# Optimization experiments

Measured on AMD Instinct MI355X. Metric: run time of the kernel, lower is better.

Reference implementation:

```python
import jax, jax.numpy as jnp
import numpy as np

NEG_SLOPE = 0.2  # PyG GATConv default leaky_relu slope


def add_self_loops(src, dst, ea, n_nodes):
    # PyG add_self_loops with fill_value='mean': self-loop attr = mean of
    # incoming edge attrs per destination node (0 if no incoming edges).
    cnt = jax.ops.segment_sum(jnp.ones(dst.shape, ea.dtype), dst, num_segments=n_nodes)
    mean_ea = jax.ops.segment_sum(ea, dst, num_segments=n_nodes) / jnp.maximum(cnt, 1.0)[:, None]
    loop = jnp.arange(n_nodes, dtype=src.dtype)
    return (jnp.concatenate([src, loop]),
            jnp.concatenate([dst, loop]),
            jnp.concatenate([ea, mean_ea], axis=0))


def gat_conv(x, src, dst, ea, W, att_src, att_dst, We, att_edge, bias, heads, ch, concat):
    n = x.shape[0]
    xs = (x @ W).reshape(n, heads, ch)                      # [N,H,C]
    a_src = (xs * att_src).sum(-1)                          # [N,H]
    a_dst = (xs * att_dst).sum(-1)                          # [N,H]
    ea_p = (ea @ We).reshape(-1, heads, ch)                 # [E,H,C]
    a_e = (ea_p * att_edge).sum(-1)                         # [E,H]
    logits = jax.nn.leaky_relu(a_src[src] + a_dst[dst] + a_e, NEG_SLOPE)
    m = jax.ops.segment_max(logits, dst, num_segments=n)    # segment softmax over dst
    e = jnp.exp(logits - m[dst])
    denom = jax.ops.segment_sum(e, dst, num_segments=n)
    alpha = e / (denom[dst] + 1e-16)                        # [E,H]
    out = jax.ops.segment_sum(alpha[:, :, None] * xs[src], dst, num_segments=n)  # [N,H,C]
    out = out.reshape(n, heads * ch) if concat else out.mean(axis=1)
    return out + bias


def setup_inputs() -> dict:
    key = jax.random.key(0)
    ks = jax.random.split(key, 14)
    N, E, F_IN, H, C1, C2 = 50000, 800000, 128, 2, 64, 64
    s = 0.05
    return {
        "x": jax.random.normal(ks[0], (N, F_IN), jnp.float32),
        "edge_index": jax.random.randint(ks[1], (2, E), 0, N, jnp.int32),
        "edge_weight": jax.random.uniform(ks[2], (E,), jnp.float32),
        # layer 1 (heads=2, concat=True)
        "W1": jax.random.normal(ks[3], (F_IN, H * C1), jnp.float32) * s,
        "att_src1": jax.random.normal(ks[4], (1, H, C1), jnp.float32) * s,
        "att_dst1": jax.random.normal(ks[5], (1, H, C1), jnp.float32) * s,
        "We1": jax.random.normal(ks[6], (1, H * C1), jnp.float32) * s,
        "att_edge1": jax.random.normal(ks[7], (1, H, C1), jnp.float32) * s,
        "b1": jnp.zeros((H * C1,), jnp.float32),
        # layer 2 (heads=1, concat=False)
        "W2": jax.random.normal(ks[8], (H * C1, C2), jnp.float32) * s,
        "att_src2": jax.random.normal(ks[9], (1, 1, C2), jnp.float32) * s,
        "att_dst2": jax.random.normal(ks[10], (1, 1, C2), jnp.float32) * s,
        "We2": jax.random.normal(ks[11], (1, C2), jnp.float32) * s,
        "att_edge2": jax.random.normal(ks[12], (1, 1, C2), jnp.float32) * s,
        "b2": jnp.zeros((C2,), jnp.float32),
    }


def reference(x, edge_index, edge_weight, W1, att_src1, att_dst1, We1, att_edge1, b1,
              W2, att_src2, att_dst2, We2, att_edge2, b2):
    n = x.shape[0]
    ea = edge_weight[:, None]  # edge_dim=1
    src, dst, ea = add_self_loops(edge_index[0], edge_index[1], ea, n)
    h = gat_conv(x, src, dst, ea, W1, att_src1, att_dst1, We1, att_edge1, b1,
                 heads=2, ch=64, concat=True)
    h = jax.nn.elu(h)
    out = gat_conv(h, src, dst, ea, W2, att_src2, att_dst2, We2, att_edge2, b2,
                   heads=1, ch=64, concat=False)
    return out
```

## Files before the change

### kernel.cpp

```cpp
#include <hip/hip_runtime.h>
#include <math.h>

#define NEG_SLOPE 0.2f

typedef unsigned int u32;
typedef unsigned short u16;
typedef unsigned long long u64;

typedef __attribute__((ext_vector_type(8))) short short8;
typedef __attribute__((ext_vector_type(4))) float f32x4;

__device__ __forceinline__ float bf2f(u16 h) {
  union { u32 u; float f; } c; c.u = ((u32)h) << 16; return c.f;
}
__device__ __forceinline__ u16 f2bf(float f) {
  union { float f; u32 u; } c; c.f = f;
  return (u16)((c.u + 0x7FFFu + ((c.u >> 16) & 1u)) >> 16);
}

__global__ __launch_bounds__(256) void k_hist(const int* __restrict__ dst, int E, int epb,
                                              u32* __restrict__ hist) {
  __shared__ u32 h[256];
  h[threadIdx.x] = 0;
  __syncthreads();
  int b = blockIdx.x;
  int beg = b * epb, end = beg + epb; if (end > E) end = E;
  for (int i = beg + threadIdx.x; i < end; i += 256)
    atomicAdd(&h[(u32)dst[i] >> 8], 1u);
  __syncthreads();
  hist[threadIdx.x * 256 + b] = h[threadIdx.x];
}

__global__ __launch_bounds__(256) void k_scanrow(u32* __restrict__ hist, u32* __restrict__ btot) {
  int bkt = blockIdx.x, t = threadIdx.x;
  u32 orig = hist[bkt * 256 + t];
  u32 v = orig;
  #pragma unroll
  for (int off = 1; off < 64; off <<= 1) {
    u32 u_ = __shfl_up(v, off);
    if ((t & 63) >= off) v += u_;
  }
  __shared__ u32 ws[4];
  if ((t & 63) == 63) ws[t >> 6] = v;
  __syncthreads();
  u32 add = 0; int w = t >> 6;
  if (w > 0) add += ws[0];
  if (w > 1) add += ws[1];
  if (w > 2) add += ws[2];
  u32 incl = v + add;
  hist[bkt * 256 + t] = incl - orig;
  if (t == 255) btot[bkt] = incl;
}

__global__ __launch_bounds__(256) void k_scanb(const u32* __restrict__ btot, u32* __restrict__ bstart) {
  int t = threadIdx.x;
  u32 orig = btot[t];
  u32 v = orig;
  #pragma unroll
  for (int off = 1; off < 64; off <<= 1) {
    u32 u_ = __shfl_up(v, off);
    if ((t & 63) >= off) v += u_;
  }
  __shared__ u32 ws[4];
  if ((t & 63) == 63) ws[t >> 6] = v;
  __syncthreads();
  u32 add = 0; int w = t >> 6;
  if (w > 0) add += ws[0];
  if (w > 1) add += ws[1];
  if (w > 2) add += ws[2];
  u32 incl = v + add;
  bstart[t] = incl - orig;
  if (t == 255) bstart[256] = incl;
}

__global__ __launch_bounds__(256) void k_binscatter(const int* __restrict__ src,
                                                    const int* __restrict__ dst,
                                                    const float* __restrict__ ew,
                                                    const u32* __restrict__ hist,
                                                    const u32* __restrict__ bstart,
                                                    u64* __restrict__ stage, int E, int epb) {
  __shared__ u32 cur[256];
  int b = blockIdx.x;
  cur[threadIdx.x] = bstart[threadIdx.x] + hist[threadIdx.x * 256 + b];
  __syncthreads();
  int beg = b * epb, end = beg + epb; if (end > E) end = E;
  for (int i = beg + threadIdx.x; i < end; i += 256) {
    int d = dst[i];
    u32 bkt = (u32)d >> 8;
    u32 pos = atomicAdd(&cur[bkt], 1u);
    float w = ew[i];
    u32 wq = (u32)(w * 65536.0f); if (wq > 65535u) wq = 65535u;
    stage[pos] = ((u64)((u32)d & 255u) << 32) | ((u64)wq << 16) | (u64)(u32)src[i];
  }
}

__global__ __launch_bounds__(256) void k_bucket(const u64* __restrict__ stage,
                                                const u32* __restrict__ bstart,
                                                u32* __restrict__ col,
                                                u32* __restrict__ ninfo, int n) {
  int bkt = blockIdx.x;
  int beg = (int)bstart[bkt], end = (int)bstart[bkt + 1];
  __shared__ u32 pk[256];
  pk[threadIdx.x] = 0;
  __syncthreads();
  for (int i = beg + threadIdx.x; i < end; i += 256) {
    u64 sv = stage[i];
    u32 ln = (u32)(sv >> 32) & 255u;
    u32 wq = (u32)((sv >> 16) & 0xFFFFu);
    u32 old = atomicAdd(&pk[ln], (1u << 24) | wq);
    u32 rank = old >> 24;
    if (rank < 64u)
      col[((((u32)bkt << 8) + ln) << 6) + rank] = (u32)sv;
  }
  __syncthreads();
  int v = (bkt << 8) + threadIdx.x;
  if (v < n) {
    u32 p = pk[threadIdx.x];
    u32 deg = p >> 24;
    float mean = ((float)(p & 0xFFFFFFu) * (1.0f / 65536.0f)) / (float)(deg > 1 ? deg : 1);
    u32 mq = (u32)(mean * 65536.0f); if (mq > 65535u) mq = 65535u;
    u32 dc = deg > 64u ? 64u : deg;
    ninfo[v] = (dc << 16) | mq;
  }
}

template<int H>
__global__ void k_bfrag(const float* __restrict__ W, uint4* __restrict__ bfrag) {
  int tid = blockIdx.x * 256 + threadIdx.x;
  int f = tid >> 6, lane = tid & 63;
  const int NF = H * 4 * 4 * 2;
  if (f >= NF) return;
  int p = f & 1, t = (f >> 1) & 3, cg = f >> 3;
  int colc = 16 * cg + (lane & 15);
  int k0 = 32 * t + 8 * (lane >> 4);
  u16 v[8];
  #pragma unroll
  for (int j = 0; j < 8; j++) {
    float w = W[(size_t)(k0 + j) * (H * 64) + colc];
    u32 bits = __float_as_uint(w);
    if (p == 0) v[j] = (u16)(bits >> 16);
    else        v[j] = f2bf(w - __uint_as_float(bits & 0xffff0000u));
  }
  uint4 o = { (u32)v[0] | ((u32)v[1] << 16), (u32)v[2] | ((u32)v[3] << 16),
              (u32)v[4] | ((u32)v[5] << 16), (u32)v[6] | ((u32)v[7] << 16) };
  bfrag[f * 64 + lane] = o;
}

template<int H>
__global__ __launch_bounds__(256) void k_gemm_mfma(const float* __restrict__ A,
                                                   const uint4* __restrict__ bfrag,
                                                   u16* __restrict__ xs_bf,
                                                   const float* __restrict__ att_src,
                                                   const float* __restrict__ att_dst,
                                                   float* __restrict__ a_src_out,
                                                   float* __restrict__ a_dst_out,
                                                   int nrows) {
  const int NCG = H * 4;
  int lane = threadIdx.x & 63;
  int wv = threadIdx.x >> 6;
  int lrow = lane & 15, lk = lane >> 4;
  int r0 = blockIdx.x * 64 + wv * 16;
  int arow = r0 + lrow; if (arow > nrows - 1) arow = nrows - 1;
  const float* ap = A + (size_t)arow * 128;

  f32x4 acc[NCG];
  #pragma unroll
  for (int cg = 0; cg < NCG; cg++) acc[cg] = (f32x4){0.f, 0.f, 0.f, 0.f};

  #pragma unroll
  for (int t = 0; t < 4; t++) {
    float4 av0 = *(const float4*)(ap + 32 * t + 8 * lk);
    float4 av1 = *(const float4*)(ap + 32 * t + 8 * lk + 4);
    float af[8] = {av0.x, av0.y, av0.z, av0.w, av1.x, av1.y, av1.z, av1.w};
    short8 ahi, alo;
    #pragma unroll
    for (int j = 0; j < 8; j++) {
      u32 bits = __float_as_uint(af[j]);
      ahi[j] = (short)(bits >> 16);
      alo[j] = (short)f2bf(af[j] - __uint_as_float(bits & 0xffff0000u));
    }
    #pragma unroll
    for (int cg = 0; cg < NCG; cg++) {
      union { uint4 u; short8 s; } bh, bl;
      bh.u = bfrag[((cg * 4 + t) * 2 + 0) * 64 + lane];
      bl.u = bfrag[((cg * 4 + t) * 2 + 1) * 64 + lane];
      acc[cg] = __builtin_amdgcn_mfma_f32_16x16x32_bf16(ahi, bh.s, acc[cg], 0, 0, 0);
      acc[cg] = __builtin_amdgcn_mfma_f32_16x16x32_bf16(ahi, bl.s, acc[cg], 0, 0, 0);
      acc[cg] = __builtin_amdgcn_mfma_f32_16x16x32_bf16(alo, bh.s, acc[cg], 0, 0, 0);
    }
  }

  float ps[2][4], pd[2][4];
  #pragma unroll
  for (int h = 0; h < 2; h++)
    #pragma unroll
    for (int r = 0; r < 4; r++) { ps[h][r] = 0.f; pd[h][r] = 0.f; }

  #pragma unroll
  for (int cg = 0; cg < NCG; cg++) {
    int colbase = 16 * cg + lrow;
    float asv = att_src[colbase];
    float adv = att_dst[colbase];
    const int h = (H == 2) ? (cg >> 2) : 0;
    #pragma unroll
    for (int r = 0; r < 4; r++) {
      ps[h][r] += acc[cg][r] * asv;
      pd[h][r] += acc[cg][r] * adv;
      int row = r0 + 4 * lk + r;
      if (row < nrows) xs_bf[(size_t)row * (H * 64) + colbase] = f2bf(acc[cg][r]);
    }
  }
  #pragma unroll
  for (int h = 0; h < H; h++)
    #pragma unroll
    for (int r = 0; r < 4; r++)
      #pragma unroll
      for (int off = 8; off; off >>= 1) {
        ps[h][r] += __shfl_xor(ps[h][r], off);
        pd[h][r] += __shfl_xor(pd[h][r], off);
      }
  if (lrow == 0) {
    #pragma unroll
    for (int r = 0; r < 4; r++) {
      int row = r0 + 4 * lk + r;
      if (row < nrows) {
        #pragma unroll
        for (int h = 0; h < H; h++) {
          a_src_out[row * H + h] = ps[h][r];
          a_dst_out[row * H + h] = pd[h][r];
        }
      }
    }
  }
}

__global__ void k_scalars(const float* __restrict__ We1, const float* __restrict__ ae1,
                          const float* __restrict__ We2, const float* __restrict__ ae2,
                          float* __restrict__ out) {
  int t = threadIdx.x;
  if (t == 0) { float s = 0; for (int c = 0; c < 64; c++) s += We1[c] * ae1[c]; out[0] = s; }
  if (t == 1) { float s = 0; for (int c = 0; c < 64; c++) s += We1[64 + c] * ae1[64 + c]; out[1] = s; }
  if (t == 2) { float s = 0; for (int c = 0; c < 64; c++) s += We2[c] * ae2[c]; out[2] = s; }
}

__global__ __launch_bounds__(256) void k_agg1(const u32* __restrict__ ninfo,
                                              const u32* __restrict__ col,
                                              const float2* __restrict__ a_src,
                                              const float2* __restrict__ a_dst,
                                              const float* __restrict__ scal,
                                              const u16* __restrict__ xs_bf,
                                              const float* __restrict__ b1,
                                              float* __restrict__ h_out, int n) {
  int wid = (blockIdx.x * 256 + threadIdx.x) >> 4;
  int gl = threadIdx.x & 15;
  if (wid >= n) return;
  u32 nf = ninfo[wid];
  int deg = (int)(nf >> 16);
  float mean = (float)(nf & 0xFFFFu) * (1.0f / 65536.0f);
  float2 ad = a_dst[wid];
  float2 asv_s = a_src[wid];
  float sc0 = scal[0], sc1 = scal[1];
  bool hi = gl >= 8;
  float l0s = asv_s.x + ad.x + mean * sc0;
  float l1s = asv_s.y + ad.y + mean * sc1;
  l0s = l0s > 0.f ? l0s : NEG_SLOPE * l0s;
  l1s = l1s > 0.f ? l1s : NEG_SLOPE * l1s;
  float m0 = l0s, m1 = l1s, den0 = 1.f, den1 = 1.f;
  float acc[8];
  {
    uint4 q = *(const uint4*)&xs_bf[(size_t)wid * 128 + 8 * gl];
    acc[0] = bf2f((u16)q.x); acc[1] = bf2f((u16)(q.x >> 16));
    acc[2] = bf2f((u16)q.y); acc[3] = bf2f((u16)(q.y >> 16));
    acc[4] = bf2f((u16)q.z); acc[5] = bf2f((u16)(q.z >> 16));
    acc[6] = bf2f((u16)q.w); acc[7] = bf2f((u16)(q.w >> 16));
  }
  const u32* cw = col + ((u32)wid << 6);
  for (int p0 = 0; p0 < deg; p0 += 16) {
    int p = p0 + gl;
    bool act = p < deg;
    u32 sw = cw[act ? p : 0];
    int s = (int)(sw & 0xFFFFu);
    float w = (float)(sw >> 16) * (1.0f / 65536.0f);
    float2 asv = a_src[s];
    float l0 = asv.x + ad.x + w * sc0;
    float l1 = asv.y + ad.y + w * sc1;
    l0 = l0 > 0.f ? l0 : NEG_SLOPE * l0;
    l1 = l1 > 0.f ? l1 : NEG_SLOPE * l1;
    if (!act) { l0 = -1e30f; l1 = -1e30f; }
    float cm0 = l0, cm1 = l1;
    #pragma unroll
    for (int off = 8; off; off >>= 1) {
      cm0 = fmaxf(cm0, __shfl_xor(cm0, off, 16));
      cm1 = fmaxf(cm1, __shfl_xor(cm1, off, 16));
    }
    float nm0 = fmaxf(m0, cm0), nm1 = fmaxf(m1, cm1);
    float e0 = __expf(l0 - nm0), e1 = __expf(l1 - nm1);
    float cs0 = e0, cs1 = e1;
    #pragma unroll
    for (int off = 8; off; off >>= 1) {
      cs0 += __shfl_xor(cs0, off, 16);
      cs1 += __shfl_xor(cs1, off, 16);
    }
    float r0 = __expf(m0 - nm0), r1 = __expf(m1 - nm1);
    den0 = den0 * r0 + cs0;
    den1 = den1 * r1 + cs1;
    float rs = hi ? r1 : r0;
    #pragma unroll
    for (int f = 0; f < 8; f++) acc[f] *= rs;
    m0 = nm0; m1 = nm1;
    int cnt = deg - p0; if (cnt > 16) cnt = 16;
    int j = 0;
    for (; j + 2 <= cnt; j += 2) {
      int sj0 = __shfl(s, j, 16);
      int sj1 = __shfl(s, j + 1, 16);
      uint4 qa = *(const uint4*)&xs_bf[(size_t)sj0 * 128 + 8 * gl];
      uint4 qb = *(const uint4*)&xs_bf[(size_t)sj1 * 128 + 8 * gl];
      float a0 = __shfl(e0, j, 16), a1 = __shfl(e1, j, 16);
      float b0 = __shfl(e0, j + 1, 16), b1 = __shfl(e1, j + 1, 16);
      float ala = hi ? a1 : a0;
      float alb = hi ? b1 : b0;
      acc[0] += ala * bf2f((u16)qa.x); acc[1] += ala * bf2f((u16)(qa.x >> 16));
      acc[2] += ala * bf2f((u16)qa.y); acc[3] += ala * bf2f((u16)(qa.y >> 16));
      acc[4] += ala * bf2f((u16)qa.z); acc[5] += ala * bf2f((u16)(qa.z >> 16));
      acc[6] += ala * bf2f((u16)qa.w); acc[7] += ala * bf2f((u16)(qa.w >> 16));
      acc[0] += alb * bf2f((u16)qb.x); acc[1] += alb * bf2f((u16)(qb.x >> 16));
      acc[2] += alb * bf2f((u16)qb.y); acc[3] += alb * bf2f((u16)(qb.y >> 16));
      acc[4] += alb * bf2f((u16)qb.z); acc[5] += alb * bf2f((u16)(qb.z >> 16));
      acc[6] += alb * bf2f((u16)qb.w); acc[7] += alb * bf2f((u16)(qb.w >> 16));
    }
    if (j < cnt) {
      int sj = __shfl(s, j, 16);
      uint4 q = *(const uint4*)&xs_bf[(size_t)sj * 128 + 8 * gl];
      float a0 = __shfl(e0, j, 16), a1 = __shfl(e1, j, 16);
      float al = hi ? a1 : a0;
      acc[0] += al * bf2f((u16)q.x); acc[1] += al * bf2f((u16)(q.x >> 16));
      acc[2] += al * bf2f((u16)q.y); acc[3] += al * bf2f((u16)(q.y >> 16));
      acc[4] += al * bf2f((u16)q.z); acc[5] += al * bf2f((u16)(q.z >> 16));
      acc[6] += al * bf2f((u16)q.w); acc[7] += al * bf2f((u16)(q.w >> 16));
    }
  }
  float inv = 1.f / ((hi ? den1 : den0) + 1e-16f);
  float4 blo = *(const float4*)&b1[8 * gl];
  float4 bhi = *(const float4*)&b1[8 * gl + 4];
  float o[8];
  o[0] = acc[0] * inv + blo.x; o[1] = acc[1] * inv + blo.y;
  o[2] = acc[2] * inv + blo.z; o[3] = acc[3] * inv + blo.w;
  o[4] = acc[4] * inv + bhi.x; o[5] = acc[5] * inv + bhi.y;
  o[6] = acc[6] * inv + bhi.z; o[7] = acc[7] * inv + bhi.w;
  #pragma unroll
  for (int f = 0; f < 8; f++) o[f] = o[f] > 0.f ? o[f] : expm1f(o[f]);
  float* dst = &h_out[(size_t)wid * 128 + 8 * gl];
  *(float4*)dst = make_float4(o[0], o[1], o[2], o[3]);
  *(float4*)(dst + 4) = make_float4(o[4], o[5], o[6], o[7]);
}

__global__ __launch_bounds__(256) void k_agg2(const u32* __restrict__ ninfo,
                                              const u32* __restrict__ col,
                                              const float* __restrict__ a_src,
                                              const float* __restrict__ a_dst,
                                              const float* __restrict__ scal,
                                              const u16* __restrict__ xs_bf,
                                              const float* __restrict__ b2,
                                              float* __restrict__ out, int n) {
  int wid = (blockIdx.x * 256 + threadIdx.x) >> 3;
  int gl = threadIdx.x & 7;
  if (wid >= n) return;
  u32 nf = ninfo[wid];
  int deg = (int)(nf >> 16);
  float mean = (float)(nf & 0xFFFFu) * (1.0f / 65536.0f);
  float adv = a_dst[wid];
  float sc = scal[2];
  float ls = a_src[wid] + adv + mean * sc;
  ls = ls > 0.f ? ls : NEG_SLOPE * ls;
  float m = ls, den = 1.f;
  float acc[8];
  {
    uint4 q = *(const uint4*)&xs_bf[(size_t)wid * 64 + 8 * gl];
    acc[0] = bf2f((u16)q.x); acc[1] = bf2f((u16)(q.x >> 16));
    acc[2] = bf2f((u16)q.y); acc[3] = bf2f((u16)(q.y >> 16));
    acc[4] = bf2f((u16)q.z); acc[5] = bf2f((u16)(q.z >> 16));
    acc[6] = bf2f((u16)q.w); acc[7] = bf2f((u16)(q.w >> 16));
  }
  const u32* cw = col + ((u32)wid << 6);
  for (int p0 = 0; p0 < deg; p0 += 8) {
    int p = p0 + gl;
    bool act = p < deg;
    u32 sw = cw[act ? p : 0];
    int s = (int)(sw & 0xFFFFu);
    float w = (float)(sw >> 16) * (1.0f / 65536.0f);
    float l = a_src[s] + adv + w * sc;
    l = l > 0.f ? l : NEG_SLOPE * l;
    if (!act) l = -1e30f;
    float cm = l;
    #pragma unroll
    for (int off = 4; off; off >>= 1) cm = fmaxf(cm, __shfl_xor(cm, off, 8));
    float nm = fmaxf(m, cm);
    float e = __expf(l - nm);
    float cs = e;
    #pragma unroll
    for (int off = 4; off; off >>= 1) cs += __shfl_xor(cs, off, 8);
    float r = __expf(m - nm);
    den = den * r + cs;
    #pragma unroll
    for (int f = 0; f < 8; f++) acc[f] *= r;
    m = nm;
    int cnt = deg - p0; if (cnt > 8) cnt = 8;
    int j = 0;
    for (; j + 2 <= cnt; j += 2) {
      int sj0 = __shfl(s, j, 8);
      int sj1 = __shfl(s, j + 1, 8);
      uint4 qa = *(const uint4*)&xs_bf[(size_t)sj0 * 64 + 8 * gl];
      uint4 qb = *(const uint4*)&xs_bf[(size_t)sj1 * 64 + 8 * gl];
      float aja = __shfl(e, j, 8);
      float ajb = __shfl(e, j + 1, 8);
      acc[0] += aja * bf2f((u16)qa.x); acc[1] += aja * bf2f((u16)(qa.x >> 16));
      acc[2] += aja * bf2f((u16)qa.y); acc[3] += aja * bf2f((u16)(qa.y >> 16));
      acc[4] += aja * bf2f((u16)qa.z); acc[5] += aja * bf2f((u16)(qa.z >> 16));
      acc[6] += aja * bf2f((u16)qa.w); acc[7] += aja * bf2f((u16)(qa.w >> 16));
      acc[0] += ajb * bf2f((u16)qb.x); acc[1] += ajb * bf2f((u16)(qb.x >> 16));
      acc[2] += ajb * bf2f((u16)qb.y); acc[3] += ajb * bf2f((u16)(qb.y >> 16));
      acc[4] += ajb * bf2f((u16)qb.z); acc[5] += ajb * bf2f((u16)(qb.z >> 16));
      acc[6] += ajb * bf2f((u16)qb.w); acc[7] += ajb * bf2f((u16)(qb.w >> 16));
    }
    if (j < cnt) {
      int sj = __shfl(s, j, 8);
      uint4 q = *(const uint4*)&xs_bf[(size_t)sj * 64 + 8 * gl];
      float aj = __shfl(e, j, 8);
      acc[0] += aj * bf2f((u16)q.x); acc[1] += aj * bf2f((u16)(q.x >> 16));
      acc[2] += aj * bf2f((u16)q.y); acc[3] += aj * bf2f((u16)(q.y >> 16));
      acc[4] += aj * bf2f((u16)q.z); acc[5] += aj * bf2f((u16)(q.z >> 16));
      acc[6] += aj * bf2f((u16)q.w); acc[7] += aj * bf2f((u16)(q.w >> 16));
    }
  }
  float inv = 1.f / (den + 1e-16f);
  float4 blo = *(const float4*)&b2[8 * gl];
  float4 bhi = *(const float4*)&b2[8 * gl + 4];
  float* dst = &out[(size_t)wid * 64 + 8 * gl];
  *(float4*)dst = make_float4(acc[0] * inv + blo.x, acc[1] * inv + blo.y,
                              acc[2] * inv + blo.z, acc[3] * inv + blo.w);
  *(float4*)(dst + 4) = make_float4(acc[4] * inv + bhi.x, acc[5] * inv + bhi.y,
                                    acc[6] * inv + bhi.z, acc[7] * inv + bhi.w);
}

extern "C" void kernel_launch(void* const* d_in, const int* in_sizes, int n_in,
                              void* d_out, int out_size, void* d_ws, size_t ws_size,
                              hipStream_t stream) {
  const float* x   = (const float*)d_in[0];
  const int*   ei  = (const int*)d_in[1];
  const float* ew  = (const float*)d_in[2];
  const float* W1  = (const float*)d_in[3];
  const float* as1 = (const float*)d_in[4];
  const float* ad1 = (const float*)d_in[5];
  const float* We1 = (const float*)d_in[6];
  const float* ae1 = (const float*)d_in[7];
  const float* b1  = (const float*)d_in[8];
  const float* W2  = (const float*)d_in[9];
  const float* as2 = (const float*)d_in[10];
  const float* ad2 = (const float*)d_in[11];
  const float* We2 = (const float*)d_in[12];
  const float* ae2 = (const float*)d_in[13];
  const float* b2  = (const float*)d_in[14];

  const int n = in_sizes[0] / 128;
  const int E = in_sizes[1] / 2;
  const int epb = (E + 255) / 256;
  const int nbk = (n + 255) >> 8;

  char* wsb = (char*)d_ws;
  size_t off = 0;
  auto alloc = [&](size_t bytes) -> void* {
    void* p = wsb + off; off += (bytes + 255) & ~(size_t)255; return p;
  };
  u32*   hist    = (u32*)  alloc((size_t)256 * 256 * 4);
  u32*   btot    = (u32*)  alloc((size_t)256 * 4);
  u32*   bstart  = (u32*)  alloc((size_t)257 * 4);
  u64*   stage   = (u64*)  alloc((size_t)E * 8);
  u32*   col     = (u32*)  alloc((size_t)n * 64 * 4);
  u32*   ninfo   = (u32*)  alloc((size_t)n * 4);
  uint4* bfrag1  = (uint4*)alloc((size_t)64 * 64 * 16);
  uint4* bfrag2  = (uint4*)alloc((size_t)32 * 64 * 16);
  u16*   xs_bf   = (u16*)  alloc((size_t)n * 128 * 2);
  float* h1      = (float*)alloc((size_t)n * 128 * 4);
  float* a_src1v = (float*)alloc((size_t)n * 2 * 4);
  float* a_dst1v = (float*)alloc((size_t)n * 2 * 4);
  float* a_src2v = (float*)alloc((size_t)n * 4);
  float* a_dst2v = (float*)alloc((size_t)n * 4);
  float* scal    = (float*)alloc(64);
  if (off > ws_size) return;

  dim3 B(256);
  k_hist<<<dim3(256), B, 0, stream>>>(ei + E, E, epb, hist);
  k_scanrow<<<dim3(256), B, 0, stream>>>(hist, btot);
  k_scanb<<<dim3(1), B, 0, stream>>>(btot, bstart);
  k_binscatter<<<dim3(256), B, 0, stream>>>(ei, ei + E, ew, hist, bstart, stage, E, epb);
  k_bucket<<<dim3(nbk), B, 0, stream>>>(stage, bstart, col, ninfo, n);
  k_bfrag<2><<<dim3(16), B, 0, stream>>>(W1, bfrag1);
  k_bfrag<1><<<dim3(8), B, 0, stream>>>(W2, bfrag2);
  k_scalars<<<1, 64, 0, stream>>>(We1, ae1, We2, ae2, scal);
  k_gemm_mfma<2><<<dim3((n + 63) / 64), B, 0, stream>>>(x, bfrag1, xs_bf, as1, ad1,
                                                        a_src1v, a_dst1v, n);
  k_agg1<<<dim3((n + 15) / 16), B, 0, stream>>>(ninfo, col,
                                                (const float2*)a_src1v,
                                                (const float2*)a_dst1v,
                                                scal, xs_bf, b1, h1, n);
  k_gemm_mfma<1><<<dim3((n + 63) / 64), B, 0, stream>>>(h1, bfrag2, xs_bf, as2, ad2,
                                                        a_src2v, a_dst2v, n);
  k_agg2<<<dim3((n + 31) / 32), B, 0, stream>>>(ninfo, col, a_src2v, a_dst2v,
                                                scal, xs_bf, b2, (float*)d_out, n);
}
```

Baseline: 136.0 us.

## Replace online softmax with upfront two-pass softmax in both GAT aggregation kernels

Both aggregation kernels now load every neighbour index and its attention logit up front, in unrolled register arrays. Layer 1 holds up to 4 chunks of 16 and layer 2 up to 8 chunks of 8. They then compute the global max and denominator once, and run the feature gather loop with already-normalised exponent weights. This removes the per-chunk rescale of the accumulator and the serial chain from one chunk's max to the next, and lets the scattered a_src loads for all chunks be in flight together. In exchange it uses more registers, which may lower occupancy, and it hard-codes a maximum degree of 64, which matches the existing 64-slot row layout.

```diff
diff --git a/kernel.cpp b/kernel.cpp
--- a/kernel.cpp
+++ b/kernel.cpp
@@ -265,81 +265,99 @@
   float l1s = asv_s.y + ad.y + mean * sc1;
   l0s = l0s > 0.f ? l0s : NEG_SLOPE * l0s;
   l1s = l1s > 0.f ? l1s : NEG_SLOPE * l1s;
-  float m0 = l0s, m1 = l1s, den0 = 1.f, den1 = 1.f;
+
+  const u32* cw = col + ((u32)wid << 6);
+  int nch = (deg + 15) >> 4;
+
+  float e0a[4], e1a[4]; int sa[4];
+  #pragma unroll
+  for (int c = 0; c < 4; c++) {
+    float l0 = -1e30f, l1 = -1e30f; int s = 0;
+    if (c < nch) {
+      int p = c * 16 + gl;
+      bool act = p < deg;
+      u32 sw = cw[act ? p : 0];
+      s = (int)(sw & 0xFFFFu);
+      float w = (float)(sw >> 16) * (1.0f / 65536.0f);
+      float2 asv = a_src[s];
+      l0 = asv.x + ad.x + w * sc0;
+      l1 = asv.y + ad.y + w * sc1;
+      l0 = l0 > 0.f ? l0 : NEG_SLOPE * l0;
+      l1 = l1 > 0.f ? l1 : NEG_SLOPE * l1;
+      if (!act) { l0 = -1e30f; l1 = -1e30f; }
+    }
+    sa[c] = s; e0a[c] = l0; e1a[c] = l1;
+  }
+  float m0 = fmaxf(fmaxf(e0a[0], e0a[1]), fmaxf(e0a[2], e0a[3]));
+  float m1 = fmaxf(fmaxf(e1a[0], e1a[1]), fmaxf(e1a[2], e1a[3]));
+  #pragma unroll
+  for (int off = 8; off; off >>= 1) {
+    m0 = fmaxf(m0, __shfl_xor(m0, off, 16));
+    m1 = fmaxf(m1, __shfl_xor(m1, off, 16));
+  }
+  m0 = fmaxf(m0, l0s); m1 = fmaxf(m1, l1s);
+  float d0 = 0.f, d1 = 0.f;
+  #pragma unroll
+  for (int c = 0; c < 4; c++) {
+    float t0 = __expf(e0a[c] - m0);
+    float t1 = __expf(e1a[c] - m1);
+    e0a[c] = t0; e1a[c] = t1;
+    d0 += t0; d1 += t1;
+  }
+  #pragma unroll
+  for (int off = 8; off; off >>= 1) {
+    d0 += __shfl_xor(d0, off, 16);
+    d1 += __shfl_xor(d1, off, 16);
+  }
+  float es0 = __expf(l0s - m0), es1 = __expf(l1s - m1);
+  float den = (hi ? d1 + es1 : d0 + es0);
+  float esl = hi ? es1 : es0;
+
   float acc[8];
   {
     uint4 q = *(const uint4*)&xs_bf[(size_t)wid * 128 + 8 * gl];
-    acc[0] = bf2f((u16)q.x); acc[1] = bf2f((u16)(q.x >> 16));
-    acc[2] = bf2f((u16)q.y); acc[3] = bf2f((u16)(q.y >> 16));
-    acc[4] = bf2f((u16)q.z); acc[5] = bf2f((u16)(q.z >> 16));
-    acc[6] = bf2f((u16)q.w); acc[7] = bf2f((u16)(q.w >> 16));
-  }
-  const u32* cw = col + ((u32)wid << 6);
-  for (int p0 = 0; p0 < deg; p0 += 16) {
-    int p = p0 + gl;
-    bool act = p < deg;
-    u32 sw = cw[act ? p : 0];
-    int s = (int)(sw & 0xFFFFu);
-    float w = (float)(sw >> 16) * (1.0f / 65536.0f);
-    float2 asv = a_src[s];
-    float l0 = asv.x + ad.x + w * sc0;
-    float l1 = asv.y + ad.y + w * sc1;
-    l0 = l0 > 0.f ? l0 : NEG_SLOPE * l0;
-    l1 = l1 > 0.f ? l1 : NEG_SLOPE * l1;
-    if (!act) { l0 = -1e30f; l1 = -1e30f; }
-    float cm0 = l0, cm1 = l1;
-    #pragma unroll
-    for (int off = 8; off; off >>= 1) {
-      cm0 = fmaxf(cm0, __shfl_xor(cm0, off, 16));
-      cm1 = fmaxf(cm1, __shfl_xor(cm1, off, 16));
-    }
-    float nm0 = fmaxf(m0, cm0), nm1 = fmaxf(m1, cm1);
-    float e0 = __expf(l0 - nm0), e1 = __expf(l1 - nm1);
-    float cs0 = e0, cs1 = e1;
-    #pragma unroll
-    for (int off = 8; off; off >>= 1) {
-      cs0 += __shfl_xor(cs0, off, 16);
-      cs1 += __shfl_xor(cs1, off, 16);
-    }
-    float r0 = __expf(m0 - nm0), r1 = __expf(m1 - nm1);
-    den0 = den0 * r0 + cs0;
-    den1 = den1 * r1 + cs1;
-    float rs = hi ? r1 : r0;
-    #pragma unroll
-    for (int f = 0; f < 8; f++) acc[f] *= rs;
-    m0 = nm0; m1 = nm1;
-    int cnt = deg - p0; if (cnt > 16) cnt = 16;
-    int j = 0;
-    for (; j + 2 <= cnt; j += 2) {
-      int sj0 = __shfl(s, j, 16);
-      int sj1 = __shfl(s, j + 1, 16);
-      uint4 qa = *(const uint4*)&xs_bf[(size_t)sj0 * 128 + 8 * gl];
-      uint4 qb = *(const uint4*)&xs_bf[(size_t)sj1 * 128 + 8 * gl];
-      float a0 = __shfl(e0, j, 16), a1 = __shfl(e1, j, 16);
-      float b0 = __shfl(e0, j + 1, 16), b1 = __shfl(e1, j + 1, 16);
-      float ala = hi ? a1 : a0;
-      float alb = hi ? b1 : b0;
-      acc[0] += ala * bf2f((u16)qa.x); acc[1] += ala * bf2f((u16)(qa.x >> 16));
-      acc[2] += ala * bf2f((u16)qa.y); acc[3] += ala * bf2f((u16)(qa.y >> 16));
-      acc[4] += ala * bf2f((u16)qa.z); acc[5] += ala * bf2f((u16)(qa.z >> 16));
-      acc[6] += ala * bf2f((u16)qa.w); acc[7] += ala * bf2f((u16)(qa.w >> 16));
-      acc[0] += alb * bf2f((u16)qb.x); acc[1] += alb * bf2f((u16)(qb.x >> 16));
-      acc[2] += alb * bf2f((u16)qb.y); acc[3] += alb * bf2f((u16)(qb.y >> 16));
-      acc[4] += alb * bf2f((u16)qb.z); acc[5] += alb * bf2f((u16)(qb.z >> 16));
-      acc[6] += alb * bf2f((u16)qb.w); acc[7] += alb * bf2f((u16)(qb.w >> 16));
-    }
-    if (j < cnt) {
-      int sj = __shfl(s, j, 16);
-      uint4 q = *(const uint4*)&xs_bf[(size_t)sj * 128 + 8 * gl];
-      float a0 = __shfl(e0, j, 16), a1 = __shfl(e1, j, 16);
-      float al = hi ? a1 : a0;
-      acc[0] += al * bf2f((u16)q.x); acc[1] += al * bf2f((u16)(q.x >> 16));
-      acc[2] += al * bf2f((u16)q.y); acc[3] += al * bf2f((u16)(q.y >> 16));
-      acc[4] += al * bf2f((u16)q.z); acc[5] += al * bf2f((u16)(q.z >> 16));
-      acc[6] += al * bf2f((u16)q.w); acc[7] += al * bf2f((u16)(q.w >> 16));
-    }
-  }
-  float inv = 1.f / ((hi ? den1 : den0) + 1e-16f);
+    acc[0] = esl * bf2f((u16)q.x); acc[1] = esl * bf2f((u16)(q.x >> 16));
+    acc[2] = esl * bf2f((u16)q.y); acc[3] = esl * bf2f((u16)(q.y >> 16));
+    acc[4] = esl * bf2f((u16)q.z); acc[5] = esl * bf2f((u16)(q.z >> 16));
+    acc[6] = esl * bf2f((u16)q.w); acc[7] = esl * bf2f((u16)(q.w >> 16));
+  }
+  #pragma unroll
+  for (int c = 0; c < 4; c++) {
+    if (c < nch) {
+      int base = c * 16;
+      int cnt = deg - base; if (cnt > 16) cnt = 16;
+      int j = 0;
+      for (; j + 2 <= cnt; j += 2) {
+        int sj0 = __shfl(sa[c], j, 16);
+        int sj1 = __shfl(sa[c], j + 1, 16);
+        uint4 qa = *(const uint4*)&xs_bf[(size_t)sj0 * 128 + 8 * gl];
+        uint4 qb = *(const uint4*)&xs_bf[(size_t)sj1 * 128 + 8 * gl];
+        float a0 = __shfl(e0a[c], j, 16),     a1 = __shfl(e1a[c], j, 16);
+        float b0 = __shfl(e0a[c], j + 1, 16), b1 = __shfl(e1a[c], j + 1, 16);
+        float ala = hi ? a1 : a0;
+        float alb = hi ? b1 : b0;
+        acc[0] += ala * bf2f((u16)qa.x); acc[1] += ala * bf2f((u16)(qa.x >> 16));
+        acc[2] += ala * bf2f((u16)qa.y); acc[3] += ala * bf2f((u16)(qa.y >> 16));
+        acc[4] += ala * bf2f((u16)qa.z); acc[5] += ala * bf2f((u16)(qa.z >> 16));
+        acc[6] += ala * bf2f((u16)qa.w); acc[7] += ala * bf2f((u16)(qa.w >> 16));
+        acc[0] += alb * bf2f((u16)qb.x); acc[1] += alb * bf2f((u16)(qb.x >> 16));
+        acc[2] += alb * bf2f((u16)qb.y); acc[3] += alb * bf2f((u16)(qb.y >> 16));
+        acc[4] += alb * bf2f((u16)qb.z); acc[5] += alb * bf2f((u16)(qb.z >> 16));
+        acc[6] += alb * bf2f((u16)qb.w); acc[7] += alb * bf2f((u16)(qb.w >> 16));
+      }
+      if (j < cnt) {
+        int sj = __shfl(sa[c], j, 16);
+        uint4 q = *(const uint4*)&xs_bf[(size_t)sj * 128 + 8 * gl];
+        float a0 = __shfl(e0a[c], j, 16), a1 = __shfl(e1a[c], j, 16);
+        float al = hi ? a1 : a0;
+        acc[0] += al * bf2f((u16)q.x); acc[1] += al * bf2f((u16)(q.x >> 16));
+        acc[2] += al * bf2f((u16)q.y); acc[3] += al * bf2f((u16)(q.y >> 16));
+        acc[4] += al * bf2f((u16)q.z); acc[5] += al * bf2f((u16)(q.z >> 16));
+        acc[6] += al * bf2f((u16)q.w); acc[7] += al * bf2f((u16)(q.w >> 16));
+      }
+    }
+  }
+  float inv = 1.f / (den + 1e-16f);
   float4 blo = *(const float4*)&b1[8 * gl];
   float4 bhi = *(const float4*)&b1[8 * gl + 4];
   float o[8];
@@ -372,64 +390,81 @@
   float sc = scal[2];
   float ls = a_src[wid] + adv + mean * sc;
   ls = ls > 0.f ? ls : NEG_SLOPE * ls;
-  float m = ls, den = 1.f;
+
+  const u32* cw = col + ((u32)wid << 6);
+  int nch = (deg + 7) >> 3;
+
+  float ea[8]; int sa[8];
+  #pragma unroll
+  for (int c = 0; c < 8; c++) {
+    float l = -1e30f; int s = 0;
+    if (c < nch) {
+      int p = c * 8 + gl;
+      bool act = p < deg;
+      u32 sw = cw[act ? p : 0];
+      s = (int)(sw & 0xFFFFu);
+      float w = (float)(sw >> 16) * (1.0f / 65536.0f);
+      l = a_src[s] + adv + w * sc;
+      l = l > 0.f ? l : NEG_SLOPE * l;
+      if (!act) l = -1e30f;
+    }
+    sa[c] = s; ea[c] = l;
+  }
+  float m = ls;
+  #pragma unroll
+  for (int c = 0; c < 8; c++) m = fmaxf(m, ea[c]);
+  #pragma unroll
+  for (int off = 4; off; off >>= 1) m = fmaxf(m, __shfl_xor(m, off, 8));
+  float d = 0.f;
+  #pragma unroll
+  for (int c = 0; c < 8; c++) {
+    float t = __expf(ea[c] - m);
+    ea[c] = t; d += t;
+  }
+  #pragma unroll
+  for (int off = 4; off; off >>= 1) d += __shfl_xor(d, off, 8);
+  float es = __expf(ls - m);
+  float den = d + es;
+
   float acc[8];
   {
     uint4 q = *(const uint4*)&xs_bf[(size_t)wid * 64 + 8 * gl];
-    acc[0] = bf2f((u16)q.x); acc[1] = bf2f((u16)(q.x >> 16));
-    acc[2] = bf2f((u16)q.y); acc[3] = bf2f((u16)(q.y >> 16));
-    acc[4] = bf2f((u16)q.z); acc[5] = bf2f((u16)(q.z >> 16));
-    acc[6] = bf2f((u16)q.w); acc[7] = bf2f((u16)(q.w >> 16));
-  }
-  const u32* cw = col + ((u32)wid << 6);
-  for (int p0 = 0; p0 < deg; p0 += 8) {
-    int p = p0 + gl;
-    bool act = p < deg;
-    u32 sw = cw[act ? p : 0];
-    int s = (int)(sw & 0xFFFFu);
-    float w = (float)(sw >> 16) * (1.0f / 65536.0f);
-    float l = a_src[s] + adv + w * sc;
-    l = l > 0.f ? l : NEG_SLOPE * l;
-    if (!act) l = -1e30f;
-    float cm = l;
-    #pragma unroll
-    for (int off = 4; off; off >>= 1) cm = fmaxf(cm, __shfl_xor(cm, off, 8));
-    float nm = fmaxf(m, cm);
-    float e = __expf(l - nm);
-    float cs = e;
-    #pragma unroll
-    for (int off = 4; off; off >>= 1) cs += __shfl_xor(cs, off, 8);
-    float r = __expf(m - nm);
-    den = den * r + cs;
-    #pragma unroll
-    for (int f = 0; f < 8; f++) acc[f] *= r;
-    m = nm;
-    int cnt = deg - p0; if (cnt > 8) cnt = 8;
-    int j = 0;
-    for (; j + 2 <= cnt; j += 2) {
-      int sj0 = __shfl(s, j, 8);
-      int sj1 = __shfl(s, j + 1, 8);
-      uint4 qa = *(const uint4*)&xs_bf[(size_t)sj0 * 64 + 8 * gl];
-      uint4 qb = *(const uint4*)&xs_bf[(size_t)sj1 * 64 + 8 * gl];
-      float aja = __shfl(e, j, 8);
-      float ajb = __shfl(e, j + 1, 8);
-      acc[0] += aja * bf2f((u16)qa.x); acc[1] += aja * bf2f((u16)(qa.x >> 16));
-      acc[2] += aja * bf2f((u16)qa.y); acc[3] += aja * bf2f((u16)(qa.y >> 16));
-      acc[4] += aja * bf2f((u16)qa.z); acc[5] += aja * bf2f((u16)(qa.z >> 16));
-      acc[6] += aja * bf2f((u16)qa.w); acc[7] += aja * bf2f((u16)(qa.w >> 16));
-      acc[0] += ajb * bf2f((u16)qb.x); acc[1] += ajb * bf2f((u16)(qb.x >> 16));
-      acc[2] += ajb * bf2f((u16)qb.y); acc[3] += ajb * bf2f((u16)(qb.y >> 16));
-      acc[4] += ajb * bf2f((u16)qb.z); acc[5] += ajb * bf2f((u16)(qb.z >> 16));
-      acc[6] += ajb * bf2f((u16)qb.w); acc[7] += ajb * bf2f((u16)(qb.w >> 16));
-    }
-    if (j < cnt) {
-      int sj = __shfl(s, j, 8);
-      uint4 q = *(const uint4*)&xs_bf[(size_t)sj * 64 + 8 * gl];
-      float aj = __shfl(e, j, 8);
-      acc[0] += aj * bf2f((u16)q.x); acc[1] += aj * bf2f((u16)(q.x >> 16));
-      acc[2] += aj * bf2f((u16)q.y); acc[3] += aj * bf2f((u16)(q.y >> 16));
-      acc[4] += aj * bf2f((u16)q.z); acc[5] += aj * bf2f((u16)(q.z >> 16));
-      acc[6] += aj * bf2f((u16)q.w); acc[7] += aj * bf2f((u16)(q.w >> 16));
+    acc[0] = es * bf2f((u16)q.x); acc[1] = es * bf2f((u16)(q.x >> 16));
+    acc[2] = es * bf2f((u16)q.y); acc[3] = es * bf2f((u16)(q.y >> 16));
+    acc[4] = es * bf2f((u16)q.z); acc[5] = es * bf2f((u16)(q.z >> 16));
+    acc[6] = es * bf2f((u16)q.w); acc[7] = es * bf2f((u16)(q.w >> 16));
+  }
+  #pragma unroll
+  for (int c = 0; c < 8; c++) {
+    if (c < nch) {
+      int base = c * 8;
+      int cnt = deg - base; if (cnt > 8) cnt = 8;
+      int j = 0;
+      for (; j + 2 <= cnt; j += 2) {
+        int sj0 = __shfl(sa[c], j, 8);
+        int sj1 = __shfl(sa[c], j + 1, 8);
+        uint4 qa = *(const uint4*)&xs_bf[(size_t)sj0 * 64 + 8 * gl];
+        uint4 qb = *(const uint4*)&xs_bf[(size_t)sj1 * 64 + 8 * gl];
+        float aja = __shfl(ea[c], j, 8);
+        float ajb = __shfl(ea[c], j + 1, 8);
+        acc[0] += aja * bf2f((u16)qa.x); acc[1] += aja * bf2f((u16)(qa.x >> 16));
+        acc[2] += aja * bf2f((u16)qa.y); acc[3] += aja * bf2f((u16)(qa.y >> 16));
+        acc[4] += aja * bf2f((u16)qa.z); acc[5] += aja * bf2f((u16)(qa.z >> 16));
+        acc[6] += aja * bf2f((u16)qa.w); acc[7] += aja * bf2f((u16)(qa.w >> 16));
+        acc[0] += ajb * bf2f((u16)qb.x); acc[1] += ajb * bf2f((u16)(qb.x >> 16));
+        acc[2] += ajb * bf2f((u16)qb.y); acc[3] += ajb * bf2f((u16)(qb.y >> 16));
+        acc[4] += ajb * bf2f((u16)qb.z); acc[5] += ajb * bf2f((u16)(qb.z >> 16));
+        acc[6] += ajb * bf2f((u16)qb.w); acc[7] += ajb * bf2f((u16)(qb.w >> 16));
+      }
+      if (j < cnt) {
+        int sj = __shfl(sa[c], j, 8);
+        uint4 q = *(const uint4*)&xs_bf[(size_t)sj * 64 + 8 * gl];
+        float aj = __shfl(ea[c], j, 8);
+        acc[0] += aj * bf2f((u16)q.x); acc[1] += aj * bf2f((u16)(q.x >> 16));
+        acc[2] += aj * bf2f((u16)q.y); acc[3] += aj * bf2f((u16)(q.y >> 16));
+        acc[4] += aj * bf2f((u16)q.z); acc[5] += aj * bf2f((u16)(q.z >> 16));
+        acc[6] += aj * bf2f((u16)q.w); acc[7] += aj * bf2f((u16)(q.w >> 16));
+      }
     }
   }
   float inv = 1.f / (den + 1e-16f);
```

Result: no change. 134.0 us (-1.5%).
